# Kernel tuning notes

Hardware: AMD Instinct MI355X
Metric: run time of the kernel (lower is better)

## Reference

```python
import jax, jax.numpy as jnp
import numpy as np

BS, L, D = 128, 256, 512
H, DK = 2, 256  # heads, head dim
EPS_BN = 1e-5


def _lin(x, W, b):
    # torch Linear: W is (out, in)
    return jnp.einsum('...i,oi->...o', x, W) + b


def _bn(x, g, b, m, v):
    # eval-mode BatchNorm over channel axis = last axis of x
    return (x - m) * (g * jax.lax.rsqrt(v + EPS_BN)) + b


def setup_inputs() -> dict:
    key = jax.random.key(0)
    ks = iter(jax.random.split(key, 64))
    rn = lambda shape, s=0.02: jax.random.normal(next(ks), shape, dtype=jnp.float32) * s
    inp = {}
    inp['cap_emb'] = jax.random.normal(next(ks), (BS, L, D), dtype=jnp.float32)
    inp['lengths'] = jax.random.randint(next(ks), (BS,), 1, L + 1, dtype=jnp.int64 if jax.config.jax_enable_x64 else jnp.int32)
    # GA linears q,k,v
    for nm in ('Wq', 'Wk', 'Wv'):
        inp[nm] = rn((D, D))
    for nm in ('bq', 'bk', 'bv'):
        inp[nm] = rn((D,))
    inp['Wfq'] = rn((DK, DK)); inp['bfq'] = rn((DK,))
    inp['Wfk'] = rn((DK, DK)); inp['bfk'] = rn((DK,))
    inp['Wfg'] = rn((2 * DK, DK)); inp['bfg'] = rn((2 * DK,))
    # BatchNorm params (eval running stats)
    for pre in ('bn1', 'bn2', 'bn3'):
        inp[pre + '_g'] = 1.0 + rn((D,), 0.1)
        inp[pre + '_b'] = rn((D,), 0.1)
        inp[pre + '_m'] = rn((D,), 0.1)
        inp[pre + '_v'] = jax.random.uniform(next(ks), (D,), minval=0.5, maxval=1.5, dtype=jnp.float32)
    # Conv1d weights, torch layout (out, in, k)
    inp['Wc2'] = rn((D, D, 2)); inp['bc2'] = rn((D,))
    inp['Wc3'] = rn((D, D, 3)); inp['bc3'] = rn((D,))
    # MLP 512 -> 1024 -> 512
    inp['Wm1'] = rn((2 * D, D)); inp['bm1'] = rn((2 * D,))
    inp['Wm2'] = rn((D, 2 * D)); inp['bm2'] = rn((D,))
    return inp


def _forward(cap_emb, Wq, bq, Wk, bk, Wv, bv, Wfq, bfq, Wfk, bfk, Wfg, bfg,
             bn1_g, bn1_b, bn1_m, bn1_v, Wc2, bc2, bn2_g, bn2_b, bn2_m, bn2_v,
             Wc3, bc3, bn3_g, bn3_b, bn3_m, bn3_v, Wm1, bm1, Wm2, bm2, lengths):
    bs, seq, dim = cap_emb.shape
    # ---- GA: gated self-attention ----
    def split_heads(x):
        return x.reshape(bs, seq, H, DK).transpose(0, 2, 1, 3)  # [bs,h,seq,dk]
    q = split_heads(_lin(cap_emb, Wq, bq))
    k = split_heads(_lin(cap_emb, Wk, bk))
    v = split_heads(_lin(cap_emb, Wv, bv))
    G = _lin(q, Wfq, bfq) * _lin(k, Wfk, bfk)
    M = jax.nn.sigmoid(_lin(G, Wfg, bfg))  # [bs,h,seq,2*dk]
    qg = q * M[..., :DK]
    kg = k * M[..., DK:]
    # torch.div(..., rounding_mode='floor') == elementwise floor of scaled scores
    scores = jnp.floor(jnp.einsum('bhqd,bhkd->bhqk', qg, kg) / jnp.sqrt(jnp.float32(DK)))
    p_attn = jax.nn.softmax(scores, axis=-1)
    x = jnp.einsum('bhqk,bhkd->bhqd', p_attn, v)
    x = x.transpose(0, 2, 1, 3).reshape(bs, seq, dim)
    # BN over features (eval), dropout is identity in eval mode
    ga_emb = cap_emb + _bn(x, bn1_g, bn1_b, bn1_m, bn1_v)
    # ---- dual conv1d branches ----
    xc = cap_emb.transpose(0, 2, 1)  # [bs, D, L]
    dn = ('NCW', 'OIW', 'NCW')
    c2 = jax.lax.conv_general_dilated(xc, Wc2, window_strides=(2,), padding='VALID', dimension_numbers=dn) + bc2[None, :, None]
    c3 = jax.lax.conv_general_dilated(xc, Wc3, window_strides=(3,), padding='VALID', dimension_numbers=dn) + bc3[None, :, None]
    f2 = jax.nn.relu(_bn(c2.transpose(0, 2, 1), bn2_g, bn2_b, bn2_m, bn2_v))
    f3 = jax.nn.relu(_bn(c3.transpose(0, 2, 1), bn3_g, bn3_b, bn3_m, bn3_v))
    ga_jw = jnp.concatenate([ga_emb, f2, f3], axis=1)
    # ---- residual MLP (dropout identity in eval) ----
    hid = jax.nn.relu(_lin(ga_jw, Wm1, bm1))
    tex_emb = _lin(hid, Wm2, bm2) + ga_jw
    # ---- length-indexed gather ----
    idx = lengths.astype(jnp.int32) - 1
    out = tex_emb[jnp.arange(bs), idx]  # [bs, D]
    # l2norm
    norm = jnp.sqrt(jnp.sum(out * out, axis=-1, keepdims=True)) + 1e-8
    return out / norm


def reference(cap_emb, lengths, Wq, bq, Wk, bk, Wv, bv, Wfq, bfq, Wfk, bfk, Wfg, bfg,
              bn1_g, bn1_b, bn1_m, bn1_v, Wc2, bc2, bn2_g, bn2_b, bn2_m, bn2_v,
              Wc3, bc3, bn3_g, bn3_b, bn3_m, bn3_v, Wm1, bm1, Wm2, bm2):
    return _forward(cap_emb, Wq, bq, Wk, bk, Wv, bv, Wfq, bfq, Wfk, bfk, Wfg, bfg,
                    bn1_g, bn1_b, bn1_m, bn1_v, Wc2, bc2, bn2_g, bn2_b, bn2_m, bn2_v,
                    Wc3, bc3, bn3_g, bn3_b, bn3_m, bn3_v, Wm1, bm1, Wm2, bm2, lengths)
```

## Files before the change

### kernel.cpp

```cpp
#include <hip/hip_runtime.h>
#include <math.h>


typedef short bf16x8 __attribute__((ext_vector_type(8)));
typedef float f32x4 __attribute__((ext_vector_type(4)));
typedef short short4v __attribute__((ext_vector_type(4)));

__device__ __forceinline__ short f2bf(float x) {
    union { float f; unsigned u; } c; c.f = x;
    unsigned r = c.u + 0x7FFFu + ((c.u >> 16) & 1u);
    return (short)(r >> 16);
}
__device__ __forceinline__ float bf2f(short h) {
    union { float f; unsigned u; } c; c.u = ((unsigned)(unsigned short)h) << 16;
    return c.f;
}
__device__ __forceinline__ void glds16(const void* g, void* l) {
    __builtin_amdgcn_global_load_lds(
        (const __attribute__((address_space(1))) void*)g,
        (__attribute__((address_space(3))) void*)l, 16, 0, 0);
}

struct PrepArgs {
    const float* src[3];
    short* dst[3];
    int n4[3];
    const float *Wq, *bq, *Wfq, *bfq, *Wk, *bk, *Wfk, *bfk;
    short *WaB, *WbB;
    float *ba, *bb;
};
__global__ __launch_bounds__(256) void prep_kernel(PrepArgs a)
{
    const int y = blockIdx.y;
    const int t = threadIdx.x;
    if (y < 3) {
        const float4* s = (const float4*)a.src[y];
        short* d = a.dst[y];
        const int n4 = a.n4[y];
        for (int i = blockIdx.x * 256 + t; i < n4; i += gridDim.x * 256) {
            float4 x = s[i];
            short4v h;
            h.x = f2bf(x.x); h.y = f2bf(x.y); h.z = f2bf(x.z); h.w = f2bf(x.w);
            *(short4v*)&d[i * 4] = h;
        }
        return;
    }
    if (blockIdx.x >= 512) return;
    __shared__ float fq[256];
    __shared__ float redc[256];
    const int op = blockIdx.x;
    const int h = op >> 8, o = op & 255;
    const bool second = (y == 4);
    const float* W  = second ? a.Wk  : a.Wq;
    const float* bv = second ? a.bk  : a.bq;
    const float* F  = second ? a.Wfk : a.Wfq;
    const float* bf = second ? a.bfk : a.bfq;
    short* WB   = second ? a.WbB : a.WaB;
    float* bout = second ? a.bb  : a.ba;

    fq[t] = F[o * 256 + t];
    redc[t] = fq[t] * bv[h * 256 + t];
    __syncthreads();
    for (int s = 128; s > 0; s >>= 1) {
        if (t < s) redc[t] += redc[t + s];
        __syncthreads();
    }
    if (t == 0) bout[op] = redc[0] + bf[o];
    float s0 = 0.f, s1 = 0.f;
    for (int d = 0; d < 256; ++d) {
        const float f = fq[d];
        const float* wr = W + (size_t)(h * 256 + d) * 512;
        s0 += f * wr[t];
        s1 += f * wr[t + 256];
    }
    const size_t ro = (size_t)op * 512;
    WB[ro + t] = f2bf(s0);
    WB[ro + 256 + t] = f2bf(s1);
}

__global__ __launch_bounds__(256)
void gemm_g_qg(const short* __restrict__ capB,
               const short* __restrict__ WaB, const short* __restrict__ WbB,
               const float* __restrict__ ba, const float* __restrict__ bb,
               short* __restrict__ Gbuf,
               const float* __restrict__ cap,
               const float* __restrict__ Wq, const float* __restrict__ bq,
               const float* __restrict__ Wfg, const float* __restrict__ bfg,
               const int* __restrict__ lengths, float* __restrict__ qg)
{
    __shared__ short lds[2][12288];
    const int tid = threadIdx.x;

    if (blockIdx.x < 256) {
        float* cr = (float*)&lds[0][0];
        float* gs = cr + 512;
        const int b = blockIdx.x >> 1, h = blockIdx.x & 1;
        const int t = tid;
        int r = lengths[b] - 1;
        if (r < 0) r = 0;
        if (r > 255) r = 255;
        const size_t base = ((size_t)b * 256 + r) * 512;
        cr[t] = cap[base + t];
        cr[t + 256] = cap[base + 256 + t];
        __syncthreads();
        {
            const bf16x8* wa8 = (const bf16x8*)(WaB + (size_t)(h * 256 + t) * 512);
            const bf16x8* wb8 = (const bf16x8*)(WbB + (size_t)(h * 256 + t) * 512);
            float sa = 0.f, sb = 0.f;
            for (int k8 = 0; k8 < 64; ++k8) {
                bf16x8 wa = wa8[k8];
                bf16x8 wb = wb8[k8];
#pragma unroll
                for (int j = 0; j < 8; ++j) {
                    const float c = cr[k8 * 8 + j];
                    sa += bf2f(wa[j]) * c;
                    sb += bf2f(wb[j]) * c;
                }
            }
            gs[t] = (sb + bb[h * 256 + t]) * (sa + ba[h * 256 + t]);
        }
        __syncthreads();
        const float4* wq4 = (const float4*)(Wq + (size_t)(h * 256 + t) * 512);
        float q = 0.f;
        for (int k4 = 0; k4 < 128; ++k4) {
            float4 w = wq4[k4];
            q += w.x * cr[k4 * 4 + 0] + w.y * cr[k4 * 4 + 1]
               + w.z * cr[k4 * 4 + 2] + w.w * cr[k4 * 4 + 3];
        }
        q += bq[h * 256 + t];
        const float4* w4 = (const float4*)(Wfg + (size_t)t * 256);
        float a = 0.f;
        for (int k4 = 0; k4 < 64; ++k4) {
            float4 w = w4[k4];
            a += w.x * gs[k4 * 4 + 0] + w.y * gs[k4 * 4 + 1]
               + w.z * gs[k4 * 4 + 2] + w.w * gs[k4 * 4 + 3];
        }
        a += bfg[t];
        qg[b * 512 + h * 256 + t] = q / (1.f + expf(-a));
        return;
    }

    const int gid = blockIdx.x - 256;
    const int bn = (gid & 1) * 128;
    const int bm = ((gid >> 1) & 255) * 128;
    const int z = gid >> 9;
    const short* B1 = WaB + (size_t)z * 256 * 512;
    const short* B2 = WbB + (size_t)z * 256 * 512;

    const int lane = tid & 63;
    const int wr = (tid >> 7) & 1, wc = (tid >> 6) & 1;
    const int fr = lane & 15, kc = lane >> 4;
    const int r0 = tid >> 2;
    const int e0 = (((tid & 3) ^ ((r0 >> 1) & 3))) * 8;
    const int kce = (kc ^ ((fr >> 1) & 3)) * 8;

    auto stage = [&](int ph, int k0) {
        short* b = lds[ph];
        glds16(capB + (size_t)(bm + r0) * 512 + k0 + e0,      b + tid * 8);
        glds16(capB + (size_t)(bm + r0 + 64) * 512 + k0 + e0, b + (tid + 256) * 8);
        glds16(B1 + (size_t)(bn + r0) * 512 + k0 + e0,        b + 4096 + tid * 8);
        glds16(B1 + (size_t)(bn + r0 + 64) * 512 + k0 + e0,   b + 4096 + (tid + 256) * 8);
        glds16(B2 + (size_t)(bn + r0) * 512 + k0 + e0,        b + 8192 + tid * 8);
        glds16(B2 + (size_t)(bn + r0 + 64) * 512 + k0 + e0,   b + 8192 + (tid + 256) * 8);
    };

    f32x4 acc1[4][4], acc2[4][4];
#pragma unroll
    for (int i = 0; i < 4; ++i)
#pragma unroll
        for (int j = 0; j < 4; ++j) {
            acc1[i][j] = (f32x4){0.f, 0.f, 0.f, 0.f};
            acc2[i][j] = (f32x4){0.f, 0.f, 0.f, 0.f};
        }

    stage(0, 0);
    __syncthreads();
    for (int s = 0; s < 16; ++s) {
        if (s + 1 < 16) stage((s + 1) & 1, (s + 1) * 32);
        const short* b = lds[s & 1];
        bf16x8 ah[4], bh[4];
#pragma unroll
        for (int i = 0; i < 4; ++i)
            ah[i] = *(const bf16x8*)&b[(wr * 64 + i * 16 + fr) * 32 + kce];
#pragma unroll
        for (int i = 0; i < 4; ++i)
            bh[i] = *(const bf16x8*)&b[4096 + (wc * 64 + i * 16 + fr) * 32 + kce];
#pragma unroll
        for (int mi = 0; mi < 4; ++mi)
#pragma unroll
            for (int ni = 0; ni < 4; ++ni)
                acc1[mi][ni] = __builtin_amdgcn_mfma_f32_16x16x32_bf16(ah[mi], bh[ni], acc1[mi][ni], 0, 0, 0);
#pragma unroll
        for (int i = 0; i < 4; ++i)
            bh[i] = *(const bf16x8*)&b[8192 + (wc * 64 + i * 16 + fr) * 32 + kce];
#pragma unroll
        for (int mi = 0; mi < 4; ++mi)
#pragma unroll
            for (int ni = 0; ni < 4; ++ni)
                acc2[mi][ni] = __builtin_amdgcn_mfma_f32_16x16x32_bf16(ah[mi], bh[ni], acc2[mi][ni], 0, 0, 0);
        __syncthreads();
    }

#pragma unroll
    for (int mi = 0; mi < 4; ++mi) {
#pragma unroll
        for (int ni = 0; ni < 4; ++ni) {
#pragma unroll
            for (int r = 0; r < 4; ++r) {
                const int row = bm + wr * 64 + mi * 16 + kc * 4 + r;
                const int col = bn + wc * 64 + ni * 16 + fr;
                const float av  = acc1[mi][ni][r] + ba[z * 256 + col];
                const float lin = acc2[mi][ni][r] + bb[z * 256 + col];
                Gbuf[(size_t)row * 512 + z * 256 + col] = f2bf(lin * av);
            }
        }
    }
}

__global__ __launch_bounds__(256, 2)
void gemm_kg(const short* __restrict__ Gbuf,
             const short* __restrict__ Wfg2B, const float* __restrict__ bias,
             const short* __restrict__ capB,
             const short* __restrict__ WkB, const float* __restrict__ bk,
             const float* __restrict__ qg, float* __restrict__ scorep)
{
    __shared__ short lds[2][16384];
    __shared__ float sp[256];
    const int tid = threadIdx.x;
    const int bm = blockIdx.y * 128;
    const int bn = blockIdx.x * 128;
    const int z = blockIdx.z;
    const short* A1 = Gbuf + (size_t)z * 256;
    const short* B2 = WkB + (size_t)z * 256 * 512;

    const int lane = tid & 63;
    const int wr = (tid >> 7) & 1, wc = (tid >> 6) & 1;
    const int fr = lane & 15, kc = lane >> 4;
    const int r0 = tid >> 2;
    const int e0 = (((tid & 3) ^ ((r0 >> 1) & 3))) * 8;
    const int kce = (kc ^ ((fr >> 1) & 3)) * 8;

    auto stage = [&](int ph, int s) {
        short* b = lds[ph];
        const int k0 = s * 32;
        glds16(capB + (size_t)(bm + r0) * 512 + k0 + e0,      b + 8192 + tid * 8);
        glds16(capB + (size_t)(bm + r0 + 64) * 512 + k0 + e0, b + 8192 + (tid + 256) * 8);
        glds16(B2 + (size_t)(bn + r0) * 512 + k0 + e0,        b + 12288 + tid * 8);
        glds16(B2 + (size_t)(bn + r0 + 64) * 512 + k0 + e0,   b + 12288 + (tid + 256) * 8);
        if (s < 8) {
            glds16(A1 + (size_t)(bm + r0) * 512 + k0 + e0,        b + tid * 8);
            glds16(A1 + (size_t)(bm + r0 + 64) * 512 + k0 + e0,   b + (tid + 256) * 8);
            glds16(Wfg2B + (size_t)(bn + r0) * 256 + k0 + e0,     b + 4096 + tid * 8);
            glds16(Wfg2B + (size_t)(bn + r0 + 64) * 256 + k0 + e0, b + 4096 + (tid + 256) * 8);
        }
    };

    f32x4 acc1[4][4], acc2[4][4];
#pragma unroll
    for (int i = 0; i < 4; ++i)
#pragma unroll
        for (int j = 0; j < 4; ++j) {
            acc1[i][j] = (f32x4){0.f, 0.f, 0.f, 0.f};
            acc2[i][j] = (f32x4){0.f, 0.f, 0.f, 0.f};
        }

    stage(0, 0);
    __syncthreads();
    for (int s = 0; s < 16; ++s) {
        if (s + 1 < 16) stage((s + 1) & 1, s + 1);
        const short* b = lds[s & 1];
        bf16x8 ah[4], bh[4];
#pragma unroll
        for (int i = 0; i < 4; ++i)
            ah[i] = *(const bf16x8*)&b[8192 + (wr * 64 + i * 16 + fr) * 32 + kce];
#pragma unroll
        for (int i = 0; i < 4; ++i)
            bh[i] = *(const bf16x8*)&b[12288 + (wc * 64 + i * 16 + fr) * 32 + kce];
#pragma unroll
        for (int mi = 0; mi < 4; ++mi)
#pragma unroll
            for (int ni = 0; ni < 4; ++ni)
                acc2[mi][ni] = __builtin_amdgcn_mfma_f32_16x16x32_bf16(ah[mi], bh[ni], acc2[mi][ni], 0, 0, 0);
        if (s < 8) {
#pragma unroll
            for (int i = 0; i < 4; ++i)
                ah[i] = *(const bf16x8*)&b[(wr * 64 + i * 16 + fr) * 32 + kce];
#pragma unroll
            for (int i = 0; i < 4; ++i)
                bh[i] = *(const bf16x8*)&b[4096 + (wc * 64 + i * 16 + fr) * 32 + kce];
#pragma unroll
            for (int mi = 0; mi < 4; ++mi)
#pragma unroll
                for (int ni = 0; ni < 4; ++ni)
                    acc1[mi][ni] = __builtin_amdgcn_mfma_f32_16x16x32_bf16(ah[mi], bh[ni], acc1[mi][ni], 0, 0, 0);
        }
        __syncthreads();
    }

    float qgv[4];
    float pt[4][4];
    {
        const int b = bm >> 8;
#pragma unroll
        for (int ni = 0; ni < 4; ++ni)
            qgv[ni] = qg[b * 512 + z * 256 + bn + wc * 64 + ni * 16 + fr];
#pragma unroll
        for (int mi = 0; mi < 4; ++mi)
#pragma unroll
            for (int r = 0; r < 4; ++r) pt[mi][r] = 0.f;
    }

#pragma unroll
    for (int mi = 0; mi < 4; ++mi) {
#pragma unroll
        for (int ni = 0; ni < 4; ++ni) {
#pragma unroll
            for (int r = 0; r < 4; ++r) {
                const int col = bn + wc * 64 + ni * 16 + fr;
                const float v = acc1[mi][ni][r] + bias[col];
                const float e = acc2[mi][ni][r] + bk[z * 256 + col];
                const float kgv = e / (1.f + expf(-v));
                pt[mi][r] += kgv * qgv[ni];
            }
        }
    }

#pragma unroll
    for (int mi = 0; mi < 4; ++mi) {
#pragma unroll
        for (int r = 0; r < 4; ++r) {
            float p = pt[mi][r];
            p += __shfl_xor(p, 1);
            p += __shfl_xor(p, 2);
            p += __shfl_xor(p, 4);
            p += __shfl_xor(p, 8);
            if (fr == 0) {
                const int row_local = wr * 64 + mi * 16 + kc * 4 + r;
                sp[row_local * 2 + wc] = p;
            }
        }
    }
    __syncthreads();
    if (tid < 128) {
        const int row = bm + tid;
        const float s = sp[tid * 2] + sp[tid * 2 + 1];
        const int b = row >> 8, j = row & 255;
        scorep[((size_t)(b * 2 + z) * 256 + j) * 2 + blockIdx.x] = s;
    }
}

__global__ __launch_bounds__(256)
void pbar_bnx(const float* __restrict__ scorep, const short* __restrict__ capB,
              const float* __restrict__ cap, const int* __restrict__ lengths,
              const float* __restrict__ Wv, const float* __restrict__ bv,
              const float* __restrict__ g1, const float* __restrict__ b1,
              const float* __restrict__ m1, const float* __restrict__ v1,
              float* __restrict__ xga)
{
    __shared__ float sc[512], red[512], pb[1024];
    const int b = blockIdx.x;
    const int t = threadIdx.x;
#pragma unroll
    for (int i = 0; i < 2; ++i) {
        const int o = t + i * 256;
        const int h = o >> 8, j = o & 255;
        const size_t si = ((size_t)(b * 2 + h) * 256 + j) * 2;
        sc[o] = floorf((scorep[si] + scorep[si + 1]) * 0.0625f);
    }
    __syncthreads();
    red[t] = sc[t]; red[t + 256] = sc[t + 256];
    __syncthreads();
    for (int s = 128; s > 0; s >>= 1) {
        if (t < s) {
            red[t] = fmaxf(red[t], red[t + s]);
            red[256 + t] = fmaxf(red[256 + t], red[256 + t + s]);
        }
        __syncthreads();
    }
    const float mx0 = red[0], mx1 = red[256];
    __syncthreads();
    const float e0 = expf(sc[t] - mx0);
    const float e1 = expf(sc[t + 256] - mx1);
    red[t] = e0; red[t + 256] = e1;
    __syncthreads();
    for (int s = 128; s > 0; s >>= 1) {
        if (t < s) { red[t] += red[t + s]; red[256 + t] += red[256 + t + s]; }
        __syncthreads();
    }
    sc[t] = e0 / red[0];
    sc[t + 256] = e1 / red[256];
    __syncthreads();

    float a00 = 0.f, a01 = 0.f, a10 = 0.f, a11 = 0.f;
    for (int j = 0; j < 256; ++j) {
        const float p0 = sc[j], p1 = sc[256 + j];
        const float cv0 = bf2f(capB[((size_t)(b * 256 + j)) * 512 + t]);
        const float cv1 = bf2f(capB[((size_t)(b * 256 + j)) * 512 + 256 + t]);
        a00 += p0 * cv0; a01 += p0 * cv1;
        a10 += p1 * cv0; a11 += p1 * cv1;
    }
    pb[t] = a00; pb[256 + t] = a01;
    pb[512 + t] = a10; pb[768 + t] = a11;
    __syncthreads();

    int r = lengths[b] - 1;
    if (r < 0) r = 0;
    if (r > 255) r = 255;
    const size_t base = ((size_t)b * 256 + r) * 512;
    float x0 = 0.f, x1 = 0.f;
    {
        const float4* w4 = (const float4*)(Wv + (size_t)t * 512);
        for (int k4 = 0; k4 < 128; ++k4) {
            float4 w = w4[k4];
            x0 += w.x * pb[k4 * 4 + 0] + w.y * pb[k4 * 4 + 1]
                + w.z * pb[k4 * 4 + 2] + w.w * pb[k4 * 4 + 3];
        }
        x0 += bv[t];
    }
    {
        const float4* w4 = (const float4*)(Wv + (size_t)(t + 256) * 512);
        for (int k4 = 0; k4 < 128; ++k4) {
            float4 w = w4[k4];
            x1 += w.x * pb[512 + k4 * 4 + 0] + w.y * pb[512 + k4 * 4 + 1]
                + w.z * pb[512 + k4 * 4 + 2] + w.w * pb[512 + k4 * 4 + 3];
        }
        x1 += bv[t + 256];
    }
    const int c0 = t, c1 = t + 256;
    const float s0 = g1[c0] / sqrtf(v1[c0] + 1e-5f);
    const float s1 = g1[c1] / sqrtf(v1[c1] + 1e-5f);
    xga[b * 512 + c0] = cap[base + c0] + (x0 - m1[c0]) * s0 + b1[c0];
    xga[b * 512 + c1] = cap[base + c1] + (x1 - m1[c1]) * s1 + b1[c1];
}

__global__ __launch_bounds__(256)
void mlp1(const float* __restrict__ xga, const float* __restrict__ W,
          const float* __restrict__ bias, float* __restrict__ hid)
{
    __shared__ float xs[16 * 512];
    const int r0 = blockIdx.y * 16;
    const int c0 = blockIdx.x * 64;
    for (int i = threadIdx.x; i < 2048; i += 256)
        ((float4*)xs)[i] = ((const float4*)(xga + (size_t)r0 * 512))[i];
    __syncthreads();
    const int col = c0 + (threadIdx.x & 63);
    const int rg = (threadIdx.x >> 6) * 4;
    float acc[4] = {0.f, 0.f, 0.f, 0.f};
    const float4* w4 = (const float4*)(W + (size_t)col * 512);
    for (int k4 = 0; k4 < 128; ++k4) {
        float4 w = w4[k4];
#pragma unroll
        for (int rr = 0; rr < 4; ++rr) {
            float4 x = *(const float4*)&xs[(rg + rr) * 512 + k4 * 4];
            acc[rr] += w.x * x.x + w.y * x.y + w.z * x.z + w.w * x.w;
        }
    }
    const float bb = bias[col];
#pragma unroll
    for (int rr = 0; rr < 4; ++rr)
        hid[(size_t)(r0 + rg + rr) * 1024 + col] = fmaxf(acc[rr] + bb, 0.f);
}

__global__ __launch_bounds__(256)
void mlp2(const float* __restrict__ hid, const float* __restrict__ W,
          const float* __restrict__ bias, const float* __restrict__ xga,
          float* __restrict__ tex)
{
    __shared__ float xs[16 * 1024];
    const int r0 = blockIdx.y * 16;
    const int c0 = blockIdx.x * 64;
    for (int i = threadIdx.x; i < 4096; i += 256)
        ((float4*)xs)[i] = ((const float4*)(hid + (size_t)r0 * 1024))[i];
    __syncthreads();
    const int col = c0 + (threadIdx.x & 63);
    const int rg = (threadIdx.x >> 6) * 4;
    float acc[4] = {0.f, 0.f, 0.f, 0.f};
    const float4* w4 = (const float4*)(W + (size_t)col * 1024);
    for (int k4 = 0; k4 < 256; ++k4) {
        float4 w = w4[k4];
#pragma unroll
        for (int rr = 0; rr < 4; ++rr) {
            float4 x = *(const float4*)&xs[(rg + rr) * 1024 + k4 * 4];
            acc[rr] += w.x * x.x + w.y * x.y + w.z * x.z + w.w * x.w;
        }
    }
    const float bb = bias[col];
#pragma unroll
    for (int rr = 0; rr < 4; ++rr) {
        const int row = r0 + rg + rr;
        tex[(size_t)row * 512 + col] = acc[rr] + bb + xga[(size_t)row * 512 + col];
    }
}

__global__ __launch_bounds__(256)
void norm_out(const float* __restrict__ tex, float* __restrict__ out)
{
    __shared__ float red[256];
    const int b = blockIdx.x;
    const int t = threadIdx.x;
    const float a = tex[b * 512 + t];
    const float c = tex[b * 512 + 256 + t];
    red[t] = a * a + c * c;
    __syncthreads();
    for (int s = 128; s > 0; s >>= 1) {
        if (t < s) red[t] += red[t + s];
        __syncthreads();
    }
    const float inv = 1.f / (sqrtf(red[0]) + 1e-8f);
    out[b * 512 + t] = a * inv;
    out[b * 512 + 256 + t] = c * inv;
}

extern "C" void kernel_launch(void* const* d_in, const int* in_sizes, int n_in,
                              void* d_out, int out_size, void* d_ws, size_t ws_size,
                              hipStream_t stream)
{
    const float* cap = (const float*)d_in[0];
    const int* lengths = (const int*)d_in[1];
    const float* Wq  = (const float*)d_in[2];
    const float* Wk  = (const float*)d_in[3];
    const float* Wv  = (const float*)d_in[4];
    const float* bq  = (const float*)d_in[5];
    const float* bk  = (const float*)d_in[6];
    const float* bv  = (const float*)d_in[7];
    const float* Wfq = (const float*)d_in[8];
    const float* bfq = (const float*)d_in[9];
    const float* Wfk = (const float*)d_in[10];
    const float* bfk = (const float*)d_in[11];
    const float* Wfg = (const float*)d_in[12];
    const float* bfg = (const float*)d_in[13];
    const float* g1  = (const float*)d_in[14];
    const float* b1  = (const float*)d_in[15];
    const float* m1  = (const float*)d_in[16];
    const float* v1  = (const float*)d_in[17];
    const float* Wm1 = (const float*)d_in[30];
    const float* bm1 = (const float*)d_in[31];
    const float* Wm2 = (const float*)d_in[32];
    const float* bm2 = (const float*)d_in[33];
    float* out = (float*)d_out;

    char* w = (char*)d_ws;
    const size_t MB = 1024 * 1024;
    short* capB = (short*)(w);
    short* Gbuf = (short*)(w + 32 * MB);
    char* wp = w + 64 * MB;
    short* WkB   = (short*)wp; wp += 524288;
    short* WaB   = (short*)wp; wp += 524288;
    short* WbB   = (short*)wp; wp += 524288;
    short* Wfg2B = (short*)wp; wp += 131072;
    float* ba     = (float*)wp; wp += 2048;
    float* bb     = (float*)wp; wp += 2048;
    float* qg     = (float*)wp; wp += 262144;
    float* scorep = (float*)wp; wp += 524288;
    float* xga    = (float*)wp; wp += 262144;
    float* hid    = (float*)wp; wp += 524288;
    float* tex    = (float*)wp; wp += 262144;

    PrepArgs pa;
    pa.src[0] = cap;          pa.dst[0] = capB;  pa.n4[0] = 4194304;
    pa.src[1] = Wk;           pa.dst[1] = WkB;   pa.n4[1] = 65536;
    pa.src[2] = Wfg + 65536;  pa.dst[2] = Wfg2B; pa.n4[2] = 16384;
    pa.Wq = Wq; pa.bq = bq; pa.Wfq = Wfq; pa.bfq = bfq;
    pa.Wk = Wk; pa.bk = bk; pa.Wfk = Wfk; pa.bfk = bfk;
    pa.WaB = WaB; pa.WbB = WbB; pa.ba = ba; pa.bb = bb;
    prep_kernel<<<dim3(4096, 5), 256, 0, stream>>>(pa);

    gemm_g_qg<<<dim3(1280), 256, 0, stream>>>(capB, WaB, WbB, ba, bb, Gbuf,
                                              cap, Wq, bq, Wfg, bfg, lengths, qg);

    gemm_kg<<<dim3(2, 256, 2), 256, 0, stream>>>(Gbuf, Wfg2B, bfg + 256,
                                                 capB, WkB, bk, qg, scorep);

    pbar_bnx<<<dim3(128), 256, 0, stream>>>(scorep, capB, cap, lengths,
                                            Wv, bv, g1, b1, m1, v1, xga);

    mlp1<<<dim3(16, 8), 256, 0, stream>>>(xga, Wm1, bm1, hid);
    mlp2<<<dim3(8, 8), 256, 0, stream>>>(hid, Wm2, bm2, xga, tex);
    norm_out<<<dim3(128), 256, 0, stream>>>(tex, out);
}
```

Baseline: 295.2 us.

## Split query-gate computation out of G GEMM and reuse computed Gbuf rows

Moves the per-batch query-gate branch out of the fused G GEMM kernel into a separate qg_kernel. The new kernel reads the gated G row from Gbuf instead of recomputing it with a 512-long bf16 dot product per thread. The GEMM kernel now uses a 3D grid and launch_bounds(256,2), which should improve occupancy and remove divergent block roles. The cost is an extra kernel launch and a serial dependency, since qg now has to wait for the whole G GEMM to finish.

```diff
diff --git a/kernel.cpp b/kernel.cpp
--- a/kernel.cpp
+++ b/kernel.cpp
@@ -78,72 +78,17 @@
     WB[ro + 256 + t] = f2bf(s1);
 }
 
-__global__ __launch_bounds__(256)
-void gemm_g_qg(const short* __restrict__ capB,
-               const short* __restrict__ WaB, const short* __restrict__ WbB,
-               const float* __restrict__ ba, const float* __restrict__ bb,
-               short* __restrict__ Gbuf,
-               const float* __restrict__ cap,
-               const float* __restrict__ Wq, const float* __restrict__ bq,
-               const float* __restrict__ Wfg, const float* __restrict__ bfg,
-               const int* __restrict__ lengths, float* __restrict__ qg)
+__global__ __launch_bounds__(256, 2)
+void gemm_g(const short* __restrict__ capB,
+            const short* __restrict__ WaB, const short* __restrict__ WbB,
+            const float* __restrict__ ba, const float* __restrict__ bb,
+            short* __restrict__ Gbuf)
 {
     __shared__ short lds[2][12288];
     const int tid = threadIdx.x;
-
-    if (blockIdx.x < 256) {
-        float* cr = (float*)&lds[0][0];
-        float* gs = cr + 512;
-        const int b = blockIdx.x >> 1, h = blockIdx.x & 1;
-        const int t = tid;
-        int r = lengths[b] - 1;
-        if (r < 0) r = 0;
-        if (r > 255) r = 255;
-        const size_t base = ((size_t)b * 256 + r) * 512;
-        cr[t] = cap[base + t];
-        cr[t + 256] = cap[base + 256 + t];
-        __syncthreads();
-        {
-            const bf16x8* wa8 = (const bf16x8*)(WaB + (size_t)(h * 256 + t) * 512);
-            const bf16x8* wb8 = (const bf16x8*)(WbB + (size_t)(h * 256 + t) * 512);
-            float sa = 0.f, sb = 0.f;
-            for (int k8 = 0; k8 < 64; ++k8) {
-                bf16x8 wa = wa8[k8];
-                bf16x8 wb = wb8[k8];
-#pragma unroll
-                for (int j = 0; j < 8; ++j) {
-                    const float c = cr[k8 * 8 + j];
-                    sa += bf2f(wa[j]) * c;
-                    sb += bf2f(wb[j]) * c;
-                }
-            }
-            gs[t] = (sb + bb[h * 256 + t]) * (sa + ba[h * 256 + t]);
-        }
-        __syncthreads();
-        const float4* wq4 = (const float4*)(Wq + (size_t)(h * 256 + t) * 512);
-        float q = 0.f;
-        for (int k4 = 0; k4 < 128; ++k4) {
-            float4 w = wq4[k4];
-            q += w.x * cr[k4 * 4 + 0] + w.y * cr[k4 * 4 + 1]
-               + w.z * cr[k4 * 4 + 2] + w.w * cr[k4 * 4 + 3];
-        }
-        q += bq[h * 256 + t];
-        const float4* w4 = (const float4*)(Wfg + (size_t)t * 256);
-        float a = 0.f;
-        for (int k4 = 0; k4 < 64; ++k4) {
-            float4 w = w4[k4];
-            a += w.x * gs[k4 * 4 + 0] + w.y * gs[k4 * 4 + 1]
-               + w.z * gs[k4 * 4 + 2] + w.w * gs[k4 * 4 + 3];
-        }
-        a += bfg[t];
-        qg[b * 512 + h * 256 + t] = q / (1.f + expf(-a));
-        return;
-    }
-
-    const int gid = blockIdx.x - 256;
-    const int bn = (gid & 1) * 128;
-    const int bm = ((gid >> 1) & 255) * 128;
-    const int z = gid >> 9;
+    const int bm = blockIdx.y * 128;
+    const int bn = blockIdx.x * 128;
+    const int z = blockIdx.z;
     const short* B1 = WaB + (size_t)z * 256 * 512;
     const short* B2 = WbB + (size_t)z * 256 * 512;
 
@@ -215,6 +160,44 @@
             }
         }
     }
+}
+
+__global__ __launch_bounds__(256)
+void qg_kernel(const float* __restrict__ cap,
+               const short* __restrict__ Gbuf,
+               const float* __restrict__ Wq, const float* __restrict__ bq,
+               const float* __restrict__ Wfg, const float* __restrict__ bfg,
+               const int* __restrict__ lengths, float* __restrict__ qg)
+{
+    __shared__ float cr[512];
+    __shared__ float gs[256];
+    const int b = blockIdx.x >> 1, h = blockIdx.x & 1;
+    const int t = threadIdx.x;
+    int r = lengths[b] - 1;
+    if (r < 0) r = 0;
+    if (r > 255) r = 255;
+    const size_t base = ((size_t)b * 256 + r) * 512;
+    cr[t] = cap[base + t];
+    cr[t + 256] = cap[base + 256 + t];
+    gs[t] = bf2f(Gbuf[base + h * 256 + t]);
+    __syncthreads();
+    const float4* wq4 = (const float4*)(Wq + (size_t)(h * 256 + t) * 512);
+    float q = 0.f;
+    for (int k4 = 0; k4 < 128; ++k4) {
+        float4 w = wq4[k4];
+        q += w.x * cr[k4 * 4 + 0] + w.y * cr[k4 * 4 + 1]
+           + w.z * cr[k4 * 4 + 2] + w.w * cr[k4 * 4 + 3];
+    }
+    q += bq[h * 256 + t];
+    const float4* w4 = (const float4*)(Wfg + (size_t)t * 256);
+    float a = 0.f;
+    for (int k4 = 0; k4 < 64; ++k4) {
+        float4 w = w4[k4];
+        a += w.x * gs[k4 * 4 + 0] + w.y * gs[k4 * 4 + 1]
+           + w.z * gs[k4 * 4 + 2] + w.w * gs[k4 * 4 + 3];
+    }
+    a += bfg[t];
+    qg[b * 512 + h * 256 + t] = q / (1.f + expf(-a));
 }
 
 __global__ __launch_bounds__(256, 2)
@@ -565,8 +548,9 @@
     pa.WaB = WaB; pa.WbB = WbB; pa.ba = ba; pa.bb = bb;
     prep_kernel<<<dim3(4096, 5), 256, 0, stream>>>(pa);
 
-    gemm_g_qg<<<dim3(1280), 256, 0, stream>>>(capB, WaB, WbB, ba, bb, Gbuf,
-                                              cap, Wq, bq, Wfg, bfg, lengths, qg);
+    gemm_g<<<dim3(2, 256, 2), 256, 0, stream>>>(capB, WaB, WbB, ba, bb, Gbuf);
+
+    qg_kernel<<<dim3(256), 256, 0, stream>>>(cap, Gbuf, Wq, bq, Wfg, bfg, lengths, qg);
 
     gemm_kg<<<dim3(2, 256, 2), 256, 0, stream>>>(Gbuf, Wfg2B, bfg + 256,
                                                  capB, WkB, bk, qg, scorep);
```

New measurement: 265.9 us. 1.11x faster.
